# Performance work log

Hardware: AMD Instinct MI355X
Metric: run time of the kernel (lower is better)

## Reference

```python
import jax, jax.numpy as jnp
import numpy as np

B, C, OC, H, W = 2, 64, 128, 96, 96
HD, DI, N, R, K = C // 2, C, 16, 2, 4  # VSSBlock: hidden=C/2, d_inner=2*hidden=C, d_state, dt_rank, 4 scan dirs
EPS = 1e-5


def _conv(x, w, b, pad, groups=1):
    y = jax.lax.conv_general_dilated(x, w, (1, 1), pad, feature_group_count=groups,
                                     dimension_numbers=('NCHW', 'OIHW', 'NCHW'))
    return y + b[None, :, None, None]


def _ln(x, w, b):
    m = x.mean(-1, keepdims=True)
    v = x.var(-1, keepdims=True)
    return (x - m) * jax.lax.rsqrt(v + EPS) * w + b


def _selective_scan(xs, dts, Bs, Cs, A, D):
    # xs, dts: (B,K,DI,L); Bs, Cs: (B,K,N,L); A: (K,DI,N); D: (K,DI)
    dts = jax.nn.softplus(dts)

    def step(h, inp):
        u_t, dt_t, B_t, C_t = inp
        dA = jnp.exp(dt_t[..., None] * A)                         # (B,K,DI,N)
        h = dA * h + (dt_t * u_t)[..., None] * B_t[:, :, None, :]
        return h, jnp.einsum('bkdn,bkn->bkd', h, C_t)

    seq = (jnp.moveaxis(xs, -1, 0), jnp.moveaxis(dts, -1, 0),
           jnp.moveaxis(Bs, -1, 0), jnp.moveaxis(Cs, -1, 0))
    h0 = jnp.zeros(xs.shape[:3] + (A.shape[-1],), xs.dtype)
    _, ys = jax.lax.scan(step, h0, seq)
    return jnp.moveaxis(ys, 0, -1) + D[None, :, :, None] * xs


def _vss_block(x, ln_w, ln_b, in_w, conv_w, conv_b, xproj_w, dtproj_w, dtproj_b,
               A_logs, Ds, on_w, on_b, out_w):
    # x: (B,H,W,HD); VMamba SS2D with 4-direction cross-scan + residual
    b, hh, ww, _ = x.shape
    L = hh * ww
    h = _ln(x, ln_w, ln_b)
    xz = h @ in_w                                   # (B,H,W,2*DI)
    xp, z = jnp.split(xz, 2, axis=-1)
    xc = jnp.transpose(xp, (0, 3, 1, 2))            # (B,DI,H,W)
    xc = jax.nn.silu(_conv(xc, conv_w, conv_b, ((1, 1), (1, 1)), groups=DI))
    x_flat = xc.reshape(b, DI, L)
    x_wh = jnp.transpose(xc, (0, 1, 3, 2)).reshape(b, DI, L)
    x2 = jnp.stack([x_flat, x_wh], axis=1)
    xs = jnp.concatenate([x2, jnp.flip(x2, -1)], axis=1)      # (B,4,DI,L)
    x_dbl = jnp.einsum('bkdl,kcd->bkcl', xs, xproj_w)
    dts, Bs, Cs = jnp.split(x_dbl, [R, R + N], axis=2)
    dts = jnp.einsum('bkrl,kdr->bkdl', dts, dtproj_w) + dtproj_b[None, :, :, None]
    A = -jnp.exp(A_logs)
    ys = _selective_scan(xs, dts, Bs, Cs, A, Ds)              # (B,4,DI,L)
    inv = jnp.flip(ys[:, 2:4], -1)
    unwh = lambda t: jnp.transpose(t.reshape(b, DI, ww, hh), (0, 1, 3, 2)).reshape(b, DI, L)
    y = ys[:, 0] + inv[:, 0] + unwh(ys[:, 1]) + unwh(inv[:, 1])
    y = jnp.transpose(y.reshape(b, DI, hh, ww), (0, 2, 3, 1))
    y = _ln(y, on_w, on_b) * jax.nn.silu(z)
    return x + y @ out_w


def _forward(x, ms_dw33_w, ms_dw33_b, ms_in_w, ms_in_b, ms_scale,
             vss_ln_w, vss_ln_b, vss_in_w, vss_conv_w, vss_conv_b, vss_xproj_w,
             vss_dtproj_w, vss_dtproj_b, vss_A_logs, vss_Ds, vss_on_w, vss_on_b, vss_out_w,
             ma_conv_w, ma_conv_b, adw_h_w, adw_h_b, adw_w_w, adw_w_b,
             pw_w, pw_b, bn_w, bn_b, bn_mean, bn_var):
    vss = (vss_ln_w, vss_ln_b, vss_in_w, vss_conv_w, vss_conv_b, vss_xproj_w,
           vss_dtproj_w, vss_dtproj_b, vss_A_logs, vss_Ds, vss_on_w, vss_on_b, vss_out_w)
    # --- MambaSplit (shared VSSBlock applied to both channel halves) ---
    xd = _conv(x, ms_dw33_w, ms_dw33_b, ((1, 1), (1, 1)), groups=C)
    x1, x2 = jnp.split(xd, 2, axis=1)

    def branch(xp):
        y = _vss_block(jnp.transpose(xp, (0, 2, 3, 1)), *vss)
        return ms_scale * xp + jnp.transpose(y, (0, 3, 1, 2))

    xm = jnp.concatenate([branch(x1), branch(x2)], axis=1)
    m = xm.mean((2, 3), keepdims=True)
    v = xm.var((2, 3), keepdims=True)
    xm = (xm - m) * jax.lax.rsqrt(v + EPS) * ms_in_w[None, :, None, None] + ms_in_b[None, :, None, None]
    xm = jax.nn.leaky_relu(xm, 0.01)
    # --- MaxAvg (global avg+max pool -> 3x3 conv on 1x1 map -> sigmoid gate) ---
    pooled = jnp.concatenate([x.mean((2, 3), keepdims=True), x.max((2, 3), keepdims=True)], axis=1)
    gate = jax.nn.sigmoid(_conv(pooled, ma_conv_w, ma_conv_b, ((1, 1), (1, 1))))
    xs_ = xm + gate * x
    # --- AxialDW ---
    xs_ = xs_ + _conv(xs_, adw_h_w, adw_h_b, ((1, 1), (0, 0)), groups=C) \
              + _conv(xs_, adw_w_w, adw_w_b, ((0, 0), (1, 1)), groups=C)
    # --- BN (eval) + ReLU, 1x1 conv, 2x2 maxpool ---
    skip = jax.nn.relu((xs_ - bn_mean[None, :, None, None]) * jax.lax.rsqrt(bn_var[None, :, None, None] + EPS)
                       * bn_w[None, :, None, None] + bn_b[None, :, None, None])
    out = _conv(skip, pw_w, pw_b, ((0, 0), (0, 0)))
    down = jax.lax.reduce_window(out, -jnp.inf, jax.lax.max, (1, 1, 2, 2), (1, 1, 2, 2), 'VALID')
    return down, skip


def setup_inputs() -> dict:
    key = jax.random.key(0)
    ks = jax.random.split(key, 16)
    r = lambda i, shape, s=0.02: jax.random.normal(ks[i], shape, jnp.float32) * s
    return {
        'x': jax.random.normal(ks[0], (B, C, H, W), jnp.float32),
        'ms_dw33_w': r(1, (C, 1, 3, 3), 0.1), 'ms_dw33_b': jnp.zeros(C),
        'ms_in_w': jnp.ones(C), 'ms_in_b': jnp.zeros(C),
        'ms_scale': jnp.ones((1,)),
        'vss_ln_w': jnp.ones(HD), 'vss_ln_b': jnp.zeros(HD),
        'vss_in_w': r(2, (HD, 2 * DI)),
        'vss_conv_w': r(3, (DI, 1, 3, 3), 0.1), 'vss_conv_b': jnp.zeros(DI),
        'vss_xproj_w': r(4, (K, R + 2 * N, DI)),
        'vss_dtproj_w': r(5, (K, DI, R), 0.1), 'vss_dtproj_b': r(6, (K, DI), 0.1),
        'vss_A_logs': jnp.tile(jnp.log(jnp.arange(1, N + 1, dtype=jnp.float32)), (K, DI, 1)),
        'vss_Ds': jnp.ones((K, DI)),
        'vss_on_w': jnp.ones(DI), 'vss_on_b': jnp.zeros(DI),
        'vss_out_w': r(7, (DI, HD)),
        'ma_conv_w': r(8, (C, 2 * C, 3, 3), 0.05), 'ma_conv_b': jnp.zeros(C),
        'adw_h_w': r(9, (C, 1, 3, 1), 0.1), 'adw_h_b': jnp.zeros(C),
        'adw_w_w': r(10, (C, 1, 1, 3), 0.1), 'adw_w_b': jnp.zeros(C),
        'pw_w': r(11, (OC, C, 1, 1)), 'pw_b': jnp.zeros(OC),
        'bn_w': jnp.ones(C), 'bn_b': jnp.zeros(C),
        'bn_mean': jnp.zeros(C), 'bn_var': jnp.ones(C),
    }


def reference(x, ms_dw33_w, ms_dw33_b, ms_in_w, ms_in_b, ms_scale,
              vss_ln_w, vss_ln_b, vss_in_w, vss_conv_w, vss_conv_b, vss_xproj_w,
              vss_dtproj_w, vss_dtproj_b, vss_A_logs, vss_Ds, vss_on_w, vss_on_b, vss_out_w,
              ma_conv_w, ma_conv_b, adw_h_w, adw_h_b, adw_w_w, adw_w_b,
              pw_w, pw_b, bn_w, bn_b, bn_mean, bn_var):
    return _forward(x, ms_dw33_w, ms_dw33_b, ms_in_w, ms_in_b, ms_scale,
                    vss_ln_w, vss_ln_b, vss_in_w, vss_conv_w, vss_conv_b, vss_xproj_w,
                    vss_dtproj_w, vss_dtproj_b, vss_A_logs, vss_Ds, vss_on_w, vss_on_b, vss_out_w,
                    ma_conv_w, ma_conv_b, adw_h_w, adw_h_b, adw_w_w, adw_w_b,
                    pw_w, pw_b, bn_w, bn_b, bn_mean, bn_var)
```

## Files before the change

### kernel.cpp

```cpp
#include <hip/hip_runtime.h>
#include <hip/hip_bf16.h>

typedef __hip_bfloat16 bf16;
#define DEV __device__ __forceinline__

constexpr int B_ = 2, C_ = 64, H_ = 96, W_ = 96, L_ = 9216;
constexpr int HD_ = 32, DI_ = 64, N_ = 16, K_ = 4, BB_ = 4;
constexpr int OC_ = 128;
constexpr int CH_ = 768, CL_ = 12;
constexpr float EPSF = 1e-5f;
constexpr int DOWN_SZ = B_ * OC_ * 48 * 48;

typedef __attribute__((ext_vector_type(8))) short short8;
typedef __attribute__((ext_vector_type(4))) float f32x4;

DEV float softplusf(float x) { return x > 15.f ? x : __logf(1.f + __expf(x)); }
DEV float b2f(bf16 v) { return __bfloat162float(v); }
DEV float lo16f(unsigned v) { return __uint_as_float(v << 16); }
DEV float hi16f(unsigned v) { return __uint_as_float(v & 0xffff0000u); }
DEV void unpk(uint4 a, uint4 b, float* v) {
  v[0] = lo16f(a.x); v[1] = hi16f(a.x); v[2] = lo16f(a.y); v[3] = hi16f(a.y);
  v[4] = lo16f(a.z); v[5] = hi16f(a.z); v[6] = lo16f(a.w); v[7] = hi16f(a.w);
  v[8] = lo16f(b.x); v[9] = hi16f(b.x); v[10] = lo16f(b.y); v[11] = hi16f(b.y);
  v[12] = lo16f(b.z); v[13] = hi16f(b.z); v[14] = lo16f(b.w); v[15] = hi16f(b.w);
}

__constant__ float kLogN[16] = {
  0.0f, 0.69314718f, 1.09861229f, 1.38629436f, 1.60943791f, 1.79175947f,
  1.94591015f, 2.07944154f, 2.19722458f, 2.30258509f, 2.39789527f,
  2.48490665f, 2.56494936f, 2.63905733f, 2.70805020f, 2.77258872f};

DEV void chunk_addr(int k, int chunk, int& idx0, int& stride) {
  int r8 = chunk & 7, q = chunk >> 3;
  if (k == 0)      { idx0 = chunk * CL_;                        stride = 1;   }
  else if (k == 1) { idx0 = (12 * r8) * 96 + q;                 stride = 96;  }
  else if (k == 2) { idx0 = L_ - 1 - chunk * CL_;               stride = -1;  }
  else             { idx0 = (95 - 12 * r8) * 96 + (95 - q);     stride = -96; }
}

DEV void pow_tree(float e1, float* ep) {
  float e2 = e1 * e1, e4 = e2 * e2, e8 = e4 * e4;
  float e3 = e2 * e1, e5 = e4 * e1, e6 = e4 * e2, e7 = e4 * e3;
  ep[0] = e1;  ep[1] = e2;  ep[2] = e3;  ep[3] = e4;
  ep[4] = e5;  ep[5] = e6;  ep[6] = e7;  ep[7] = e8;
  ep[8] = e8 * e1;  ep[9] = e8 * e2;  ep[10] = e8 * e3;  ep[11] = e8 * e4;
  ep[12] = e8 * e5; ep[13] = e8 * e6; ep[14] = e8 * e7;  ep[15] = e8 * e8;
}

DEV void ld_bu(const float* __restrict__ bB, const bf16* __restrict__ xcb, int d, int idx,
               uint4& qb0, uint4& qb1, float& t0, float& t1, float& u) {
  int uix = __builtin_amdgcn_readfirstlane(idx);
  const float* p = bB + (size_t)uix * 12;
  qb0 = *(const uint4*)p; qb1 = *(const uint4*)(p + 4);
  t0 = p[8]; t1 = p[9];
  u = b2f(xcb[(size_t)idx * DI_ + d]);
}
DEV void ld_bcu(const float* __restrict__ bB, const bf16* __restrict__ bC,
                const bf16* __restrict__ xcb, int d, int idx,
                uint4& qb0, uint4& qb1, uint4& qc0, uint4& qc1,
                float& t0, float& t1, float& u) {
  int uix = __builtin_amdgcn_readfirstlane(idx);
  const float* p = bB + (size_t)uix * 12;
  qb0 = *(const uint4*)p; qb1 = *(const uint4*)(p + 4);
  t0 = p[8]; t1 = p[9];
  const uint4* cq = (const uint4*)(bC + (size_t)uix * 16);
  qc0 = cq[0]; qc1 = cq[1];
  u = b2f(xcb[(size_t)idx * DI_ + d]);
}

__global__ void k_dw33(const float* __restrict__ x, const float* __restrict__ w,
                       const float* __restrict__ bias, float* __restrict__ out) {
  int t = blockIdx.x * 256 + threadIdx.x;
  if (t >= B_ * C_ * L_) return;
  int wi = t % W_, hi = (t / W_) % H_, c = (t / L_) % C_;
  float acc = bias[c];
#pragma unroll
  for (int dy = -1; dy <= 1; dy++) {
    int hh = hi + dy; if (hh < 0 || hh >= H_) continue;
#pragma unroll
    for (int dx = -1; dx <= 1; dx++) {
      int ww = wi + dx; if (ww < 0 || ww >= W_) continue;
      acc = fmaf(x[t + dy * W_ + dx], w[c * 9 + (dy + 1) * 3 + (dx + 1)], acc);
    }
  }
  out[t] = acc;
}

__global__ __launch_bounds__(256, 4) void k_ln_inproj(
    const float* __restrict__ xd, const float* __restrict__ lnw,
    const float* __restrict__ lnb, const float* __restrict__ inw,
    float* __restrict__ xzA, bf16* __restrict__ xzBh) {
  int bb = blockIdx.y, t = threadIdx.x;
  int b = bb & 1, co = (bb >> 1) * HD_;
  int idx0 = blockIdx.x * 64;
  __shared__ float xds[32 * 68];
  __shared__ float meanA[64], rstdA[64];
  int lane = t & 63;
  for (int r = 0; r < 8; r++) {
    int c = r * 4 + (t >> 6);
    xds[c * 68 + lane] = xd[(size_t)(b * C_ + co + c) * L_ + idx0 + lane];
  }
  __syncthreads();
  if (t < 64) {
    float s = 0.f, sq = 0.f;
#pragma unroll
    for (int c = 0; c < 32; c++) { float v = xds[c * 68 + t]; s += v; sq = fmaf(v, v, sq); }
    float mean = s * (1.f / HD_);
    float var = sq * (1.f / HD_) - mean * mean;
    meanA[t] = mean; rstdA[t] = rsqrtf(var + EPSF);
  }
  __syncthreads();
  for (int i = t; i < 2048; i += 256) {
    int c = i >> 6, idx = i & 63;
    float v = xds[c * 68 + idx];
    xds[c * 68 + idx] = (v - meanA[idx]) * rstdA[idx] * lnw[c] + lnb[c];
  }
  __syncthreads();
  int oc = t & 127, g = t >> 7;
  float acc[32];
#pragma unroll
  for (int j = 0; j < 32; j++) acc[j] = 0.f;
  for (int c = 0; c < 32; c++) {
    float wv = inw[c * 128 + oc];
    const float4* row = reinterpret_cast<const float4*>(&xds[c * 68 + g * 32]);
#pragma unroll
    for (int j4 = 0; j4 < 8; j4++) {
      float4 xv = row[j4];
      acc[j4 * 4 + 0] = fmaf(xv.x, wv, acc[j4 * 4 + 0]);
      acc[j4 * 4 + 1] = fmaf(xv.y, wv, acc[j4 * 4 + 1]);
      acc[j4 * 4 + 2] = fmaf(xv.z, wv, acc[j4 * 4 + 2]);
      acc[j4 * 4 + 3] = fmaf(xv.w, wv, acc[j4 * 4 + 3]);
    }
  }
  int occ = oc & 63;
  if (oc < 64) {
#pragma unroll
    for (int j = 0; j < 32; j++)
      xzA[(size_t)(bb * L_ + idx0 + g * 32 + j) * 64 + occ] = acc[j];
  } else {
#pragma unroll
    for (int j = 0; j < 32; j++)
      xzBh[(size_t)(bb * L_ + idx0 + g * 32 + j) * 64 + occ] = __float2bfloat16(acc[j]);
  }
}

__global__ void k_dwsilu(const float* __restrict__ xzA, const float* __restrict__ cw,
                         const float* __restrict__ cb, bf16* __restrict__ xch) {
  int t = blockIdx.x * 256 + threadIdx.x;
  int d = t & 63, idx = (t >> 6) % L_, bb = t / (L_ * DI_);
  int wi = idx % W_, hi = idx / W_;
  float acc = cb[d];
#pragma unroll
  for (int dy = -1; dy <= 1; dy++) {
    int hh = hi + dy; if (hh < 0 || hh >= H_) continue;
#pragma unroll
    for (int dx = -1; dx <= 1; dx++) {
      int ww = wi + dx; if (ww < 0 || ww >= W_) continue;
      acc = fmaf(xzA[(size_t)(bb * L_ + hh * W_ + ww) * 64 + d],
                 cw[d * 9 + (dy + 1) * 3 + (dx + 1)], acc);
    }
  }
  acc = acc / (1.f + __expf(-acc));
  xch[t] = __float2bfloat16(acc);
}

__global__ void k_wprep(const float* __restrict__ xpw, const float* __restrict__ alog,
                        bf16* __restrict__ wh, float* __restrict__ aux) {
  int i = blockIdx.x * 256 + threadIdx.x;
  if (i < 144 * 64) {
    int n = i >> 6;
    wh[i] = __float2bfloat16(n < 136 ? xpw[i] : 0.f);
  }
  if (blockIdx.x == 0 && threadIdx.x < 256) {
    int kd = threadIdx.x;
    const float* al = alog + kd * N_;
    float a0 = al[0];
    bool lin = true;
#pragma unroll
    for (int n = 1; n < N_; n++) lin = lin && (fabsf(al[n] - a0 - kLogN[n]) < 3e-5f);
    aux[kd] = -__expf(a0);
    aux[256 + kd] = lin ? 1.f : 0.f;
#pragma unroll
    for (int n = 0; n < N_; n++) aux[512 + kd * N_ + n] = -__expf(al[n]);
  }
}

__global__ __launch_bounds__(256, 4) void k_xdbl_mfma(
    const bf16* __restrict__ xch, const bf16* __restrict__ wh,
    float* __restrict__ xdblB, bf16* __restrict__ xdblC) {
  int w = threadIdx.x >> 6, lane = threadIdx.x & 63;
  int bb = blockIdx.y;
  int mtile = blockIdx.x * 4 + w;
  int idx0 = mtile * 16;
  int m = lane & 15, quad = lane >> 4;
  const bf16* arow = xch + ((size_t)bb * L_ + idx0 + m) * 64 + quad * 8;
  short8 a0 = *reinterpret_cast<const short8*>(arow);
  short8 a1 = *reinterpret_cast<const short8*>(arow + 32);
#pragma unroll
  for (int nt = 0; nt < 9; nt++) {
    int n = nt * 16 + m;
    const bf16* brow = wh + n * 64 + quad * 8;
    short8 b0 = *reinterpret_cast<const short8*>(brow);
    short8 b1 = *reinterpret_cast<const short8*>(brow + 32);
    f32x4 acc = {0.f, 0.f, 0.f, 0.f};
    acc = __builtin_amdgcn_mfma_f32_16x16x32_bf16(a0, b0, acc, 0, 0, 0);
    acc = __builtin_amdgcn_mfma_f32_16x16x32_bf16(a1, b1, acc, 0, 0, 0);
    if (n < 136) {
      int k4 = (n >= 102) ? 3 : (n >= 68) ? 2 : (n >= 34) ? 1 : 0;
      int c = n - k4 * 34;
      size_t row = (size_t)(bb * K_ + k4) * L_ + idx0 + quad * 4;
      if (c < 2) {
        float* db = xdblB + row * 12 + 8 + c;
        db[0] = acc[0]; db[12] = acc[1]; db[24] = acc[2]; db[36] = acc[3];
      } else if (c < 18) {
        bf16* bp = (bf16*)(xdblB + row * 12) + (c - 2);
        bp[0] = __float2bfloat16(acc[0]);  bp[24] = __float2bfloat16(acc[1]);
        bp[48] = __float2bfloat16(acc[2]); bp[72] = __float2bfloat16(acc[3]);
      } else {
        bf16* cp = xdblC + row * 16 + (c - 18);
        cp[0] = __float2bfloat16(acc[0]);  cp[16] = __float2bfloat16(acc[1]);
        cp[32] = __float2bfloat16(acc[2]); cp[48] = __float2bfloat16(acc[3]);
      }
    }
  }
}

__global__ __launch_bounds__(256, 4) void k_scan1(
    const float* __restrict__ xdblB, const bf16* __restrict__ xch,
    const float* __restrict__ dtw, const float* __restrict__ dtb,
    const float* __restrict__ aux, bf16* __restrict__ hbuf,
    float* __restrict__ ssum) {
  int w = threadIdx.x >> 6, d = threadIdx.x & 63;
  int chunk = blockIdx.x * 4 + w, k = blockIdx.y, bb = blockIdx.z;
  float w0 = dtw[(k * DI_ + d) * 2 + 0], w1 = dtw[(k * DI_ + d) * 2 + 1];
  float bia = dtb[k * DI_ + d];
  float A1 = aux[k * 64 + d];
  bool chain = (__ballot(aux[256 + k * 64 + d] > 0.5f) == ~0ull);
  float h[N_];
#pragma unroll
  for (int n = 0; n < N_; n++) h[n] = 0.f;
  int idx0, stride;
  chunk_addr(k, chunk, idx0, stride);
  const float* bB = xdblB + (size_t)(bb * K_ + k) * L_ * 12;
  const bf16* xcb = xch + (size_t)bb * L_ * DI_;
  float S = 0.f;
  if (chain) {
    int idx = idx0;
#pragma unroll 2
    for (int s = 0; s < CL_; s++) {
      uint4 qb0, qb1; float t0, t1, u;
      ld_bu(bB, xcb, d, idx, qb0, qb1, t0, t1, u);
      float Bv[16];
      unpk(qb0, qb1, Bv);
      float dt = softplusf(fmaf(t0, w0, fmaf(t1, w1, bia)));
      S += dt;
      float du = dt * u;
      float ep[16];
      pow_tree(__expf(dt * A1), ep);
#pragma unroll
      for (int n = 0; n < N_; n++) h[n] = fmaf(ep[n], h[n], du * Bv[n]);
      idx += stride;
    }
  } else {
    float A[N_];
#pragma unroll
    for (int n = 0; n < N_; n++) A[n] = aux[512 + (k * 64 + d) * N_ + n];
    int idx = idx0;
    for (int s = 0; s < CL_; s++) {
      uint4 qb0, qb1; float t0, t1, u;
      ld_bu(bB, xcb, d, idx, qb0, qb1, t0, t1, u);
      float Bv[16];
      unpk(qb0, qb1, Bv);
      float dt = softplusf(fmaf(t0, w0, fmaf(t1, w1, bia)));
      S += dt;
      float du = dt * u;
#pragma unroll
      for (int n = 0; n < N_; n++) h[n] = fmaf(__expf(dt * A[n]), h[n], du * Bv[n]);
      idx += stride;
    }
  }
  size_t base = (size_t)((bb * K_ + k) * CH_ + chunk) * DI_ + d;
  ssum[base] = S;
#pragma unroll
  for (int n = 0; n < N_; n++) hbuf[base * N_ + n] = __float2bfloat16(h[n]);
}

__global__ __launch_bounds__(256, 1) void k_scan2(
    const float* __restrict__ aux, const float* __restrict__ ssum,
    bf16* __restrict__ hbuf) {
  int t = blockIdx.x * 256 + threadIdx.x;
  int n = t & 15, d = (t >> 4) & 63, kk = (t >> 10) & 3, bb = t >> 12;
  float A = aux[512 + (kk * 64 + d) * N_ + n];
  size_t row = (size_t)(bb * K_ + kk) * CH_ * DI_ + d;
  constexpr int U = 32;
  float Sb[U], hb[U];
#pragma unroll
  for (int j = 0; j < U; j++) {
    size_t sb = row + (size_t)j * DI_;
    Sb[j] = ssum[sb]; hb[j] = b2f(hbuf[sb * N_ + n]);
  }
  float hp = 0.f;
  for (int c = 0; c < CH_; c += U) {
    float S2[U], h2[U];
    if (c + U < CH_) {
#pragma unroll
      for (int j = 0; j < U; j++) {
        size_t sb = row + (size_t)(c + U + j) * DI_;
        S2[j] = ssum[sb]; h2[j] = b2f(hbuf[sb * N_ + n]);
      }
    } else {
#pragma unroll
      for (int j = 0; j < U; j++) { S2[j] = 0.f; h2[j] = 0.f; }
    }
#pragma unroll
    for (int j = 0; j < U; j++) {
      size_t sb = row + (size_t)(c + j) * DI_;
      float e = __expf(A * Sb[j]);
      hbuf[sb * N_ + n] = __float2bfloat16(hp);
      hp = fmaf(e, hp, hb[j]);
    }
#pragma unroll
    for (int j = 0; j < U; j++) { Sb[j] = S2[j]; hb[j] = h2[j]; }
  }
}

__global__ __launch_bounds__(256, 4) void k_scan3(
    const float* __restrict__ xdblB, const bf16* __restrict__ xdblC,
    const bf16* __restrict__ xch, const float* __restrict__ dtw,
    const float* __restrict__ dtb, const float* __restrict__ Dsw,
    const float* __restrict__ aux, const bf16* __restrict__ hbuf,
    bf16* __restrict__ ydir) {
  int w = threadIdx.x >> 6, d = threadIdx.x & 63;
  int chunk = blockIdx.x * 4 + w, k = blockIdx.y, bb = blockIdx.z;
  float w0 = dtw[(k * DI_ + d) * 2 + 0], w1 = dtw[(k * DI_ + d) * 2 + 1];
  float bia = dtb[k * DI_ + d];
  float Dk = Dsw[k * DI_ + d];
  float A1 = aux[k * 64 + d];
  bool chain = (__ballot(aux[256 + k * 64 + d] > 0.5f) == ~0ull);
  float h[N_];
  size_t base = (size_t)((bb * K_ + k) * CH_ + chunk) * DI_ + d;
  {
    const bf16* hb = hbuf + base * N_;
    uint4 qh0 = *(const uint4*)hb, qh1 = *(const uint4*)(hb + 8);
    unpk(qh0, qh1, h);
  }
  int idx0, stride;
  chunk_addr(k, chunk, idx0, stride);
  const float* bB = xdblB + (size_t)(bb * K_ + k) * L_ * 12;
  const bf16* bC = xdblC + (size_t)(bb * K_ + k) * L_ * 16;
  const bf16* xcb = xch + (size_t)bb * L_ * DI_;
  bf16* yb = ydir + (size_t)(bb * K_ + k) * L_ * DI_;
  if (chain) {
    int idx = idx0;
#pragma unroll 2
    for (int s = 0; s < CL_; s++) {
      uint4 qb0, qb1, qc0, qc1; float t0, t1, u;
      ld_bcu(bB, bC, xcb, d, idx, qb0, qb1, qc0, qc1, t0, t1, u);
      float Bv[16], Cv[16];
      unpk(qb0, qb1, Bv); unpk(qc0, qc1, Cv);
      float dt = softplusf(fmaf(t0, w0, fmaf(t1, w1, bia)));
      float du = dt * u;
      float ep[16];
      pow_tree(__expf(dt * A1), ep);
      float m[16];
#pragma unroll
      for (int n = 0; n < N_; n++) {
        h[n] = fmaf(ep[n], h[n], du * Bv[n]);
        m[n] = h[n] * Cv[n];
      }
      float a0 = m[0] + m[1], a1 = m[2] + m[3], a2 = m[4] + m[5], a3 = m[6] + m[7];
      float a4 = m[8] + m[9], a5 = m[10] + m[11], a6 = m[12] + m[13], a7 = m[14] + m[15];
      float b0 = a0 + a1, b1 = a2 + a3, b2 = a4 + a5, b3 = a6 + a7;
      float y = fmaf(Dk, u, (b0 + b1) + (b2 + b3));
      yb[(size_t)idx * DI_ + d] = __float2bfloat16(y);
      idx += stride;
    }
  } else {
    float A[N_];
#pragma unroll
    for (int n = 0; n < N_; n++) A[n] = aux[512 + (k * 64 + d) * N_ + n];
    int idx = idx0;
    for (int s = 0; s < CL_; s++) {
      uint4 qb0, qb1, qc0, qc1; float t0, t1, u;
      ld_bcu(bB, bC, xcb, d, idx, qb0, qb1, qc0, qc1, t0, t1, u);
      float Bv[16], Cv[16];
      unpk(qb0, qb1, Bv); unpk(qc0, qc1, Cv);
      float dt = softplusf(fmaf(t0, w0, fmaf(t1, w1, bia)));
      float du = dt * u;
      float y = 0.f;
#pragma unroll
      for (int n = 0; n < N_; n++) {
        h[n] = fmaf(__expf(dt * A[n]), h[n], du * Bv[n]);
        y = fmaf(h[n], Cv[n], y);
      }
      y = fmaf(Dk, u, y);
      yb[(size_t)idx * DI_ + d] = __float2bfloat16(y);
      idx += stride;
    }
  }
}

__global__ void k_combine(const bf16* __restrict__ ydir, const bf16* __restrict__ xzBh,
                          const float* __restrict__ xd, const float* __restrict__ onw,
                          const float* __restrict__ onb, const float* __restrict__ outw,
                          const float* __restrict__ mssc, float* __restrict__ xm) {
  int w = threadIdx.x >> 6, d = threadIdx.x & 63;
  int idx = blockIdx.x * 4 + w, bb = blockIdx.y;
  int b = bb & 1, co = (bb >> 1) * HD_;
  const bf16* yd = ydir + (size_t)bb * K_ * L_ * DI_;
  size_t off = (size_t)idx * DI_ + d;
  float y = b2f(yd[off]) + b2f(yd[(size_t)L_ * DI_ + off])
          + b2f(yd[(size_t)2 * L_ * DI_ + off]) + b2f(yd[(size_t)3 * L_ * DI_ + off]);
  float s = y, sq = y * y;
#pragma unroll
  for (int m = 1; m < 64; m <<= 1) { s += __shfl_xor(s, m, 64); sq += __shfl_xor(sq, m, 64); }
  float mean = s * (1.f / DI_);
  float var = sq * (1.f / DI_) - mean * mean;
  float rstd = rsqrtf(var + EPSF);
  float yn = (y - mean) * rstd * onw[d] + onb[d];
  float z = b2f(xzBh[(size_t)(bb * L_ + idx) * 64 + d]);
  float g = yn * (z / (1.f + __expf(-z)));
  __shared__ float gs[4][DI_];
  gs[w][d] = g;
  __syncthreads();
  if (d < HD_) {
    float acc = 0.f;
#pragma unroll
    for (int dd = 0; dd < DI_; dd++) acc = fmaf(gs[w][dd], outw[dd * HD_ + d], acc);
    size_t xi = (size_t)(b * C_ + co + d) * L_ + idx;
    float xp = xd[xi];
    xm[xi] = mssc[0] * xp + xp + acc;
  }
}

__global__ __launch_bounds__(1024) void k_stats(
    const float* __restrict__ xm, const float* __restrict__ x,
    float* __restrict__ inm, float* __restrict__ inr,
    float* __restrict__ xmean, float* __restrict__ xmax) {
  int bc = blockIdx.x, t = threadIdx.x;
  const float* pm = xm + (size_t)bc * L_;
  const float* px = x + (size_t)bc * L_;
  float s = 0.f, sq = 0.f, xs = 0.f, mx = -1e30f;
  for (int i = t; i < L_; i += 1024) {
    float v = pm[i]; s += v; sq = fmaf(v, v, sq);
    float xv = px[i]; xs += xv; mx = fmaxf(mx, xv);
  }
  __shared__ float red[64];
#pragma unroll
  for (int m = 1; m < 64; m <<= 1) {
    s += __shfl_xor(s, m, 64); sq += __shfl_xor(sq, m, 64);
    xs += __shfl_xor(xs, m, 64); mx = fmaxf(mx, __shfl_xor(mx, m, 64));
  }
  int wid = t >> 6;
  if ((t & 63) == 0) { red[wid] = s; red[16 + wid] = sq; red[32 + wid] = xs; red[48 + wid] = mx; }
  __syncthreads();
  if (t == 0) {
    s = 0.f; sq = 0.f; xs = 0.f; mx = -1e30f;
#pragma unroll
    for (int i = 0; i < 16; i++) {
      s += red[i]; sq += red[16 + i]; xs += red[32 + i]; mx = fmaxf(mx, red[48 + i]);
    }
    float mean = s * (1.f / L_);
    float var = sq * (1.f / L_) - mean * mean;
    inm[bc] = mean;
    inr[bc] = rsqrtf(var + EPSF);
    xmean[bc] = xs * (1.f / L_);
    xmax[bc] = mx;
  }
}

__global__ void k_xs(const float* __restrict__ xm, const float* __restrict__ inm,
                     const float* __restrict__ inr, const float* __restrict__ msw,
                     const float* __restrict__ msb, const float* __restrict__ xmean,
                     const float* __restrict__ xmax, const float* __restrict__ maw,
                     const float* __restrict__ mab, const float* __restrict__ x,
                     float* __restrict__ xs2) {
  int t = blockIdx.x * 256 + threadIdx.x;
  int bc = t / L_, c = bc & 63, b = bc >> 6;
  __shared__ float gsh;
  if (threadIdx.x < 64) {
    int ic = threadIdx.x;
    float p = xmean[b * 64 + ic] * maw[(c * 128 + ic) * 9 + 4]
            + xmax[b * 64 + ic] * maw[(c * 128 + 64 + ic) * 9 + 4];
#pragma unroll
    for (int m = 1; m < 64; m <<= 1) p += __shfl_xor(p, m, 64);
    if (ic == 0) gsh = 1.f / (1.f + __expf(-(p + mab[c])));
  }
  __syncthreads();
  float gate = gsh;
  float v = xm[t];
  v = (v - inm[bc]) * inr[bc] * msw[c] + msb[c];
  v = v > 0.f ? v : 0.01f * v;
  xs2[t] = v + gate * x[t];
}

__global__ void k_axbn(const float* __restrict__ xs2, const float* __restrict__ hw,
                       const float* __restrict__ hb, const float* __restrict__ wwt,
                       const float* __restrict__ wb, const float* __restrict__ bnw,
                       const float* __restrict__ bnb, const float* __restrict__ bnm,
                       const float* __restrict__ bnv, float* __restrict__ skipo) {
  int t = blockIdx.x * 256 + threadIdx.x;
  if (t >= B_ * C_ * L_) return;
  int wi = t % W_, hi = (t / W_) % H_, c = (t / L_) % C_;
  float a = xs2[t];
  float hacc = hb[c];
#pragma unroll
  for (int dy = -1; dy <= 1; dy++) {
    int hh = hi + dy; if (hh < 0 || hh >= H_) continue;
    hacc = fmaf(xs2[t + dy * W_], hw[c * 3 + dy + 1], hacc);
  }
  float wacc = wb[c];
#pragma unroll
  for (int dx = -1; dx <= 1; dx++) {
    int ww = wi + dx; if (ww < 0 || ww >= W_) continue;
    wacc = fmaf(xs2[t + dx], wwt[c * 3 + dx + 1], wacc);
  }
  float v = a + hacc + wacc;
  float sv = (v - bnm[c]) * rsqrtf(bnv[c] + EPSF) * bnw[c] + bnb[c];
  skipo[t] = fmaxf(sv, 0.f);
}

__global__ void k_pwpool(const float* __restrict__ skipo, const float* __restrict__ pww,
                         const float* __restrict__ pwb, float* __restrict__ down) {
  int h2 = blockIdx.x, b = blockIdx.y, t = threadIdx.x;
  int oc0 = blockIdx.z * 32;
  __shared__ float sk[64 * 192];
  for (int i = t; i < 64 * 192; i += 256) {
    int c = i / 192, rw = i % 192, r = rw / 96, wcol = rw % 96;
    sk[i] = skipo[((size_t)(b * C_ + c) * H_ + (2 * h2 + r)) * W_ + wcol];
  }
  __syncthreads();
  for (int o = t; o < 32 * 48; o += 256) {
    int oc = oc0 + o / 48, w2 = o % 48;
    float s0 = 0.f, s1 = 0.f, s2 = 0.f, s3 = 0.f;
#pragma unroll 8
    for (int c = 0; c < 64; c++) {
      float wv = pww[oc * 64 + c];
      const float* sp = &sk[c * 192 + 2 * w2];
      s0 = fmaf(sp[0], wv, s0);
      s1 = fmaf(sp[1], wv, s1);
      s2 = fmaf(sp[96], wv, s2);
      s3 = fmaf(sp[97], wv, s3);
    }
    float v = fmaxf(fmaxf(s0, s1), fmaxf(s2, s3)) + pwb[oc];
    down[((size_t)(b * OC_ + oc) * 48 + h2) * 48 + w2] = v;
  }
}

extern "C" void kernel_launch(void* const* d_in, const int* in_sizes, int n_in,
                              void* d_out, int out_size, void* d_ws, size_t ws_size,
                              hipStream_t stream) {
  const float* x     = (const float*)d_in[0];
  const float* dw33w = (const float*)d_in[1];
  const float* dw33b = (const float*)d_in[2];
  const float* msw   = (const float*)d_in[3];
  const float* msb   = (const float*)d_in[4];
  const float* mssc  = (const float*)d_in[5];
  const float* lnw   = (const float*)d_in[6];
  const float* lnb   = (const float*)d_in[7];
  const float* inw   = (const float*)d_in[8];
  const float* cw    = (const float*)d_in[9];
  const float* cb    = (const float*)d_in[10];
  const float* xpw   = (const float*)d_in[11];
  const float* dtw   = (const float*)d_in[12];
  const float* dtb   = (const float*)d_in[13];
  const float* alog  = (const float*)d_in[14];
  const float* Dsw   = (const float*)d_in[15];
  const float* onw   = (const float*)d_in[16];
  const float* onb   = (const float*)d_in[17];
  const float* outw  = (const float*)d_in[18];
  const float* maw   = (const float*)d_in[19];
  const float* mab   = (const float*)d_in[20];
  const float* ahw   = (const float*)d_in[21];
  const float* ahb   = (const float*)d_in[22];
  const float* aww   = (const float*)d_in[23];
  const float* awb   = (const float*)d_in[24];
  const float* pww   = (const float*)d_in[25];
  const float* pwb   = (const float*)d_in[26];
  const float* bnw   = (const float*)d_in[27];
  const float* bnb   = (const float*)d_in[28];
  const float* bnm   = (const float*)d_in[29];
  const float* bnv   = (const float*)d_in[30];

  float* ws = (float*)d_ws;
  float* xd    = ws;
  float* hreg  = xd + 1179648;
  bf16*  hbuf  = (bf16*)hreg;
  float* xzA   = hreg;
  bf16*  xzBh  = (bf16*)(hreg + 6291456);
  float* xdblB = hreg + 6291456 + 1179648;
  bf16*  xdblC = (bf16*)(xdblB + 1769472);
  float* ssum  = xdblB + 1769472 + 1179648;
  bf16*  ydir  = (bf16*)(ssum + 786432);
  float* xmR   = ssum + 786432 + 4718592;
  bf16*  xch   = (bf16*)xmR;
  float* xm    = xmR;
  float* xs2   = (float*)ydir;
  float* st    = xmR + 1179648;
  float* inm = st, *inr = st + 128, *xmean = st + 256, *xmaxv = st + 384;
  float* aux   = st + 512;
  bf16*  wh    = (bf16*)(aux + 4608);

  float* outp = (float*)d_out;
  float* down = outp;
  float* skipo = outp + DOWN_SZ;

  dim3 b256(256);
  int nEl = B_ * C_ * L_;

  k_wprep<<<dim3(36), b256, 0, stream>>>(xpw, alog, wh, aux);
  k_dw33<<<dim3((nEl + 255) / 256), b256, 0, stream>>>(x, dw33w, dw33b, xd);
  k_ln_inproj<<<dim3(L_ / 64, BB_), b256, 0, stream>>>(xd, lnw, lnb, inw, xzA, xzBh);
  k_dwsilu<<<dim3(BB_ * L_ * DI_ / 256), b256, 0, stream>>>(xzA, cw, cb, xch);
  k_xdbl_mfma<<<dim3(L_ / 64, BB_), b256, 0, stream>>>(xch, wh, xdblB, xdblC);
  k_scan1<<<dim3(CH_ / 4, K_, BB_), b256, 0, stream>>>(xdblB, xch, dtw, dtb, aux, hbuf, ssum);
  k_scan2<<<dim3(BB_ * K_ * DI_ * N_ / 256), b256, 0, stream>>>(aux, ssum, hbuf);
  k_scan3<<<dim3(CH_ / 4, K_, BB_), b256, 0, stream>>>(xdblB, xdblC, xch, dtw, dtb, Dsw,
                                                      aux, hbuf, ydir);
  k_combine<<<dim3(L_ / 4, BB_), b256, 0, stream>>>(ydir, xzBh, xd, onw, onb, outw, mssc, xm);
  k_stats<<<dim3(B_ * C_), dim3(1024), 0, stream>>>(xm, x, inm, inr, xmean, xmaxv);
  k_xs<<<dim3((nEl + 255) / 256), b256, 0, stream>>>(xm, inm, inr, msw, msb, xmean, xmaxv, maw, mab, x, xs2);
  k_axbn<<<dim3((nEl + 255) / 256), b256, 0, stream>>>(xs2, ahw, ahb, aww, awb, bnw, bnb, bnm, bnv, skipo);
  k_pwpool<<<dim3(48, B_, 4), b256, 0, stream>>>(skipo, pww, pwb, down);
}
```

Baseline: 337.4 us.

## Split inter-chunk scan into segmented two-level scan for more parallelism

```diff
diff --git a/kernel.cpp b/kernel.cpp
--- a/kernel.cpp
+++ b/kernel.cpp
@@ -8,6 +8,7 @@
 constexpr int HD_ = 32, DI_ = 64, N_ = 16, K_ = 4, BB_ = 4;
 constexpr int OC_ = 128;
 constexpr int CH_ = 768, CL_ = 12;
+constexpr int SEGN = 16, SEGC = 48;
 constexpr float EPSF = 1e-5f;
 constexpr int DOWN_SZ = B_ * OC_ * 48 * 48;
 
@@ -285,42 +286,44 @@
   for (int n = 0; n < N_; n++) hbuf[base * N_ + n] = __float2bfloat16(h[n]);
 }
 
-__global__ __launch_bounds__(256, 1) void k_scan2(
+__global__ __launch_bounds__(256, 4) void k_scan2a(
     const float* __restrict__ aux, const float* __restrict__ ssum,
-    bf16* __restrict__ hbuf) {
+    bf16* __restrict__ hbuf, float* __restrict__ cumS,
+    float* __restrict__ segH, float* __restrict__ segS) {
+  int t = blockIdx.x * 256 + threadIdx.x;
+  int n = t & 15, d = (t >> 4) & 63, kk = (t >> 10) & 3, bb = (t >> 12) & 3, seg = t >> 14;
+  float A = aux[512 + (kk * 64 + d) * N_ + n];
+  size_t row = (size_t)(bb * K_ + kk) * CH_ * DI_ + d;
+  float hp = 0.f, Sc = 0.f;
+#pragma unroll 4
+  for (int j = 0; j < SEGC; j++) {
+    int c = seg * SEGC + j;
+    size_t sb = row + (size_t)c * DI_;
+    float S = ssum[sb];
+    float hl = b2f(hbuf[sb * N_ + n]);
+    hbuf[sb * N_ + n] = __float2bfloat16(hp);
+    if (n == 0) cumS[sb] = Sc;
+    hp = fmaf(__expf(A * S), hp, hl);
+    Sc += S;
+  }
+  size_t sbase = (size_t)(bb * K_ + kk) * SEGN + seg;
+  segH[(sbase * DI_ + d) * N_ + n] = hp;
+  if (n == 0) segS[sbase * DI_ + d] = Sc;
+}
+
+__global__ void k_scan2b(const float* __restrict__ aux, float* __restrict__ segH,
+                         const float* __restrict__ segS) {
   int t = blockIdx.x * 256 + threadIdx.x;
   int n = t & 15, d = (t >> 4) & 63, kk = (t >> 10) & 3, bb = t >> 12;
   float A = aux[512 + (kk * 64 + d) * N_ + n];
-  size_t row = (size_t)(bb * K_ + kk) * CH_ * DI_ + d;
-  constexpr int U = 32;
-  float Sb[U], hb[U];
-#pragma unroll
-  for (int j = 0; j < U; j++) {
-    size_t sb = row + (size_t)j * DI_;
-    Sb[j] = ssum[sb]; hb[j] = b2f(hbuf[sb * N_ + n]);
-  }
   float hp = 0.f;
-  for (int c = 0; c < CH_; c += U) {
-    float S2[U], h2[U];
-    if (c + U < CH_) {
-#pragma unroll
-      for (int j = 0; j < U; j++) {
-        size_t sb = row + (size_t)(c + U + j) * DI_;
-        S2[j] = ssum[sb]; h2[j] = b2f(hbuf[sb * N_ + n]);
-      }
-    } else {
-#pragma unroll
-      for (int j = 0; j < U; j++) { S2[j] = 0.f; h2[j] = 0.f; }
-    }
-#pragma unroll
-    for (int j = 0; j < U; j++) {
-      size_t sb = row + (size_t)(c + j) * DI_;
-      float e = __expf(A * Sb[j]);
-      hbuf[sb * N_ + n] = __float2bfloat16(hp);
-      hp = fmaf(e, hp, hb[j]);
-    }
-#pragma unroll
-    for (int j = 0; j < U; j++) { Sb[j] = S2[j]; hb[j] = h2[j]; }
+  for (int seg = 0; seg < SEGN; seg++) {
+    size_t sbase = (size_t)(bb * K_ + kk) * SEGN + seg;
+    size_t si = (sbase * DI_ + d) * N_ + n;
+    float H = segH[si];
+    float E = __expf(A * segS[sbase * DI_ + d]);
+    segH[si] = hp;
+    hp = fmaf(E, hp, H);
   }
 }
 
@@ -329,6 +332,7 @@
     const bf16* __restrict__ xch, const float* __restrict__ dtw,
     const float* __restrict__ dtb, const float* __restrict__ Dsw,
     const float* __restrict__ aux, const bf16* __restrict__ hbuf,
+    const float* __restrict__ cumS, const float* __restrict__ segH,
     bf16* __restrict__ ydir) {
   int w = threadIdx.x >> 6, d = threadIdx.x & 63;
   int chunk = blockIdx.x * 4 + w, k = blockIdx.y, bb = blockIdx.z;
@@ -339,10 +343,26 @@
   bool chain = (__ballot(aux[256 + k * 64 + d] > 0.5f) == ~0ull);
   float h[N_];
   size_t base = (size_t)((bb * K_ + k) * CH_ + chunk) * DI_ + d;
+  int seg = chunk / SEGC;
+  size_t sbase = (size_t)(bb * K_ + k) * SEGN + seg;
+  float Sc = cumS[base];
   {
     const bf16* hb = hbuf + base * N_;
     uint4 qh0 = *(const uint4*)hb, qh1 = *(const uint4*)(hb + 8);
     unpk(qh0, qh1, h);
+    const float* Hin = segH + (sbase * DI_ + d) * N_;
+    if (chain) {
+      float ep[16];
+      pow_tree(__expf(A1 * Sc), ep);
+#pragma unroll
+      for (int n = 0; n < N_; n++) h[n] = fmaf(ep[n], Hin[n], h[n]);
+    } else {
+#pragma unroll
+      for (int n = 0; n < N_; n++) {
+        float A = aux[512 + (k * 64 + d) * N_ + n];
+        h[n] = fmaf(__expf(A * Sc), Hin[n], h[n]);
+      }
+    }
   }
   int idx0, stride;
   chunk_addr(k, chunk, idx0, stride);
@@ -600,6 +620,9 @@
   float* inm = st, *inr = st + 128, *xmean = st + 256, *xmaxv = st + 384;
   float* aux   = st + 512;
   bf16*  wh    = (bf16*)(aux + 4608);
+  float* cumS  = aux + 4608 + 4608;
+  float* segH  = cumS + 786432;
+  float* segS  = segH + 262144;
 
   float* outp = (float*)d_out;
   float* down = outp;
@@ -614,9 +637,10 @@
   k_dwsilu<<<dim3(BB_ * L_ * DI_ / 256), b256, 0, stream>>>(xzA, cw, cb, xch);
   k_xdbl_mfma<<<dim3(L_ / 64, BB_), b256, 0, stream>>>(xch, wh, xdblB, xdblC);
   k_scan1<<<dim3(CH_ / 4, K_, BB_), b256, 0, stream>>>(xdblB, xch, dtw, dtb, aux, hbuf, ssum);
-  k_scan2<<<dim3(BB_ * K_ * DI_ * N_ / 256), b256, 0, stream>>>(aux, ssum, hbuf);
+  k_scan2a<<<dim3(BB_ * K_ * SEGN * DI_ * N_ / 256), b256, 0, stream>>>(aux, ssum, hbuf, cumS, segH, segS);
+  k_scan2b<<<dim3(BB_ * K_ * DI_ * N_ / 256), b256, 0, stream>>>(aux, segH, segS);
   k_scan3<<<dim3(CH_ / 4, K_, BB_), b256, 0, stream>>>(xdblB, xdblC, xch, dtw, dtb, Dsw,
-                                                      aux, hbuf, ydir);
+                                                      aux, hbuf, cumS, segH, ydir);
   k_combine<<<dim3(L_ / 4, BB_), b256, 0, stream>>>(ydir, xzBh, xd, onw, onb, outw, mssc, xm);
   k_stats<<<dim3(B_ * C_), dim3(1024), 0, stream>>>(xm, x, inm, inr, xmean, xmaxv);
   k_xs<<<dim3((nEl + 255) / 256), b256, 0, stream>>>(xm, inm, inr, msw, msb, xmean, xmaxv, maw, mab, x, xs2);
```

Result: faster. 321.0 us (-4.9%).
